# Performance work log

Hardware: AMD Instinct MI355X
Metric: run time of the kernel (lower is better)

Reference implementation:

```python
import jax, jax.numpy as jnp
import numpy as np

N_PAPER, N_AUTHOR = 200000, 100000
D_PAPER, D_AUTHOR = 128, 64
H, OUT = 64, 32
E_CITES, E_WRITES = 4000000, 2000000


def _gcn(x, W, b, src, dst, n):
    # GCNConv with default add_self_loops=True, symmetric normalization
    xl = x @ W
    deg = jnp.zeros((n,), xl.dtype).at[dst].add(1.0) + 1.0  # +1 for self loop
    dis = jax.lax.rsqrt(deg)
    norm = dis[src] * dis[dst]
    out = jax.ops.segment_sum(xl[src] * norm[:, None], dst, num_segments=n)
    out = out + xl * (dis * dis)[:, None]  # self-loop term: norm_ii = 1/deg_i
    return out + b


def _sage(x_src, x_dst, Wl, bl, Wr, src, dst, n_dst):
    # SAGEConv: mean neighbor aggregation -> lin_l, plus root lin_r on dst
    ones = jnp.ones(src.shape, x_src.dtype)
    cnt = jnp.maximum(jax.ops.segment_sum(ones, dst, num_segments=n_dst), 1.0)
    mean = jax.ops.segment_sum(x_src[src], dst, num_segments=n_dst) / cnt[:, None]
    return mean @ Wl + bl + x_dst @ Wr


def _gat(x_src, x_dst, Ws, Wd, a_s, a_d, b, src, dst, n_dst):
    # GATConv heads=1, bipartite, add_self_loops=False, leaky_relu slope 0.2
    xs = x_src @ Ws  # [Ns, H]
    xd = x_dst @ Wd  # [Nd, H]
    a_src = xs @ a_s  # [Ns]
    a_dst = xd @ a_d  # [Nd]
    e = a_src[src] + a_dst[dst]
    e = jnp.where(e > 0, e, 0.2 * e)
    m = jax.ops.segment_max(e, dst, num_segments=n_dst)
    m = jnp.where(jnp.isfinite(m), m, 0.0)  # nodes with no in-edges
    ex = jnp.exp(e - m[dst])
    denom = jax.ops.segment_sum(ex, dst, num_segments=n_dst)
    alpha = ex / denom[dst]
    out = jax.ops.segment_sum(alpha[:, None] * xs[src], dst, num_segments=n_dst)
    return out + b


def _forward(x_paper, x_author, params, cites_src, cites_dst, writes_src, writes_dst):
    for (gW, gb, sWl, sbl, sWr, aWs, aWd, aas, aad, ab) in params:
        p_gcn = _gcn(x_paper, gW, gb, cites_src, cites_dst, N_PAPER)
        p_sage = _sage(x_author, x_paper, sWl, sbl, sWr, writes_src, writes_dst, N_PAPER)
        # rev_writes: paper -> author, i.e. src=writes_dst (paper), dst=writes_src (author)
        a_gat = _gat(x_paper, x_author, aWs, aWd, aas, aad, ab, writes_dst, writes_src, N_AUTHOR)
        x_paper = jax.nn.relu(p_gcn + p_sage)  # HeteroConv aggr='sum'
        x_author = jax.nn.relu(a_gat)
    return x_paper, x_author


def setup_inputs() -> dict:
    key = jax.random.key(0)
    ks = jax.random.split(key, 40)
    rn = lambda i, shp, s=0.1: jax.random.normal(ks[i], shp, jnp.float32) * s
    inp = {}
    inp['x_paper'] = rn(0, (N_PAPER, D_PAPER), 1.0)
    inp['x_author'] = rn(1, (N_AUTHOR, D_AUTHOR), 1.0)
    dims = [(D_PAPER, D_AUTHOR), (H, H)]
    i = 2
    for l, (dp, da) in enumerate(dims):
        inp[f'gcn_W{l}'] = rn(i, (dp, H)); i += 1
        inp[f'gcn_b{l}'] = jnp.zeros((H,), jnp.float32)
        inp[f'sage_Wl{l}'] = rn(i, (da, H)); i += 1
        inp[f'sage_bl{l}'] = jnp.zeros((H,), jnp.float32)
        inp[f'sage_Wr{l}'] = rn(i, (dp, H)); i += 1
        inp[f'gat_Ws{l}'] = rn(i, (dp, H)); i += 1
        inp[f'gat_Wd{l}'] = rn(i, (da, H)); i += 1
        inp[f'gat_as{l}'] = rn(i, (H,)); i += 1
        inp[f'gat_ad{l}'] = rn(i, (H,)); i += 1
        inp[f'gat_b{l}'] = jnp.zeros((H,), jnp.float32)
    inp['lin_W'] = rn(i, (H, OUT)); i += 1
    inp['lin_b'] = jnp.zeros((OUT,), jnp.float32)
    inp['cites_src'] = jax.random.randint(ks[30], (E_CITES,), 0, N_PAPER)
    inp['cites_dst'] = jax.random.randint(ks[31], (E_CITES,), 0, N_PAPER)
    inp['writes_src'] = jax.random.randint(ks[32], (E_WRITES,), 0, N_AUTHOR)
    inp['writes_dst'] = jax.random.randint(ks[33], (E_WRITES,), 0, N_PAPER)
    return inp


def reference(x_paper, x_author,
              gcn_W0, gcn_b0, sage_Wl0, sage_bl0, sage_Wr0,
              gat_Ws0, gat_Wd0, gat_as0, gat_ad0, gat_b0,
              gcn_W1, gcn_b1, sage_Wl1, sage_bl1, sage_Wr1,
              gat_Ws1, gat_Wd1, gat_as1, gat_ad1, gat_b1,
              lin_W, lin_b,
              cites_src, cites_dst, writes_src, writes_dst):
    params = [
        (gcn_W0, gcn_b0, sage_Wl0, sage_bl0, sage_Wr0, gat_Ws0, gat_Wd0, gat_as0, gat_ad0, gat_b0),
        (gcn_W1, gcn_b1, sage_Wl1, sage_bl1, sage_Wr1, gat_Ws1, gat_Wd1, gat_as1, gat_ad1, gat_b1),
    ]
    _, x_author_out = _forward(x_paper, x_author, params, cites_src, cites_dst, writes_src, writes_dst)
    return x_author_out @ lin_W + lin_b
```

## Files before the change

kernel.cpp:

```cpp
#include <hip/hip_runtime.h>
#include <hip/hip_bf16.h>

#define NP 200000
#define NA 100000
#define DP 128
#define HD 64
#define EC 4000000
#define EW 2000000
#define NSCAN (2 * NP + NA)
#define NBUCK 8
#define CAPC 64
#define CAPW 48
#define CAPA 64

typedef __hip_bfloat16 bf16;
typedef __attribute__((ext_vector_type(8))) short short8;
typedef __attribute__((ext_vector_type(4))) float f32x4;

__device__ __forceinline__ float bf2f(bf16 h) { return __bfloat162float(h); }

__device__ __forceinline__ short8 pack8(float4 a, float4 b) {
    union {
        short8 s;
        unsigned u[4];
    } r;
    __hip_bfloat162 h;
    h = __float22bfloat162_rn(float2{a.x, a.y});
    r.u[0] = *reinterpret_cast<unsigned*>(&h);
    h = __float22bfloat162_rn(float2{a.z, a.w});
    r.u[1] = *reinterpret_cast<unsigned*>(&h);
    h = __float22bfloat162_rn(float2{b.x, b.y});
    r.u[2] = *reinterpret_cast<unsigned*>(&h);
    h = __float22bfloat162_rn(float2{b.z, b.w});
    r.u[3] = *reinterpret_cast<unsigned*>(&h);
    return r.s;
}


__global__ __launch_bounds__(256) void fill_pass_kernel(const int* __restrict__ cs,
                                                        const int* __restrict__ cd,
                                                        const int* __restrict__ ws,
                                                        const int* __restrict__ wd,
                                                        int* __restrict__ CUR,
                                                        int* __restrict__ colC,
                                                        int* __restrict__ colWd,
                                                        int* __restrict__ colWa, int bucket) {
    long i = (long)blockIdx.x * 256 + threadIdx.x;
    if (i < EC) {
        int d = __builtin_nontemporal_load(&cd[i]);
        if ((int)(((long)d * NBUCK) / NP) != bucket) return;
        int s = __builtin_nontemporal_load(&cs[i]);
        int pos = atomicAdd(&CUR[d * 4], 1);
        if (pos < CAPC) colC[(size_t)d * CAPC + pos] = s;
    } else if (i < (long)EC + EW) {
        long e = i - EC;
        int d = __builtin_nontemporal_load(&wd[e]);
        int a = __builtin_nontemporal_load(&ws[e]);
        if ((int)(((long)d * NBUCK) / NP) == bucket) {
            int pos = atomicAdd(&CUR[(NP + d) * 4], 1);
            if (pos < CAPW) colWd[(size_t)d * CAPW + pos] = a;
        }
        if ((int)(((long)a * NBUCK) / NA) == bucket) {
            int pos = atomicAdd(&CUR[(2 * NP + a) * 4], 1);
            if (pos < CAPA) colWa[(size_t)a * CAPA + pos] = d;
        }
    }
}

__global__ __launch_bounds__(256) void finalize_kernel(const int* __restrict__ CUR,
                                                       float* __restrict__ dis,
                                                       float* __restrict__ invc) {
    int i = blockIdx.x * 256 + threadIdx.x;
    if (i >= NP) return;
    dis[i] = rsqrtf((float)CUR[i * 4] + 1.0f);
    invc[i] = 1.0f / fmaxf((float)CUR[(NP + i) * 4], 1.0f);
}


__global__ __launch_bounds__(256) void conv_author_kernel(const float* __restrict__ XA,
                                                          const float* __restrict__ wvec,
                                                          bf16* __restrict__ XAbf,
                                                          float* __restrict__ adst) {
    __shared__ float vs[64];
    if (threadIdx.x < 64) vs[threadIdx.x] = wvec[threadIdx.x];
    __syncthreads();
    int r = blockIdx.x * 4 + (threadIdx.x >> 6);
    int lane = threadIdx.x & 63;
    float x = XA[(size_t)r * 64 + lane];
    XAbf[(size_t)r * 64 + lane] = __float2bfloat16(x);
    float p = x * vs[lane];
#pragma unroll
    for (int o = 32; o > 0; o >>= 1) p += __shfl_xor(p, o, 64);
    if (lane == 0) adst[r] = p;
}


__global__ void wprep_kernel(const float* __restrict__ Wg, const float* __restrict__ Wl,
                             const float* __restrict__ Wr, const float* __restrict__ Ws0,
                             const float* __restrict__ Ws1, short* __restrict__ WF) {
    int bid = blockIdx.x;
    int lane = threadIdx.x;
    int q = lane & 15, g = lane >> 4;
    int m, r;
    size_t dst;
    if (bid < 16) {
        m = 0; r = bid; dst = 0;
    } else if (bid < 40) {
        m = 1; r = bid - 16; dst = 8192;
    } else if (bid < 56) {
        m = 2; r = bid - 40; dst = 20480;
    } else {
        m = 3; r = bid - 56; dst = 28672;
    }
    int ks = r >> 2, n = r & 3;
    int col = n * 16 + q;
    float v[8];
#pragma unroll
    for (int j = 0; j < 8; j++) {
        int kr = ks * 32 + g * 8 + j;
        float x;
        if (m == 0) x = Wg[(size_t)kr * 64 + col];
        else if (m == 1) x = (kr < 64) ? Wl[(size_t)kr * 64 + col] : Wr[(size_t)(kr - 64) * 64 + col];
        else if (m == 2) x = Ws0[(size_t)kr * 64 + col];
        else x = Ws1[(size_t)kr * 64 + col];
        v[j] = x;
    }
    short8 s = pack8(float4{v[0], v[1], v[2], v[3]}, float4{v[4], v[5], v[6], v[7]});
    *reinterpret_cast<short8*>(WF + dst + ((size_t)r * 64 + lane) * 8) = s;
}


template <int K, bool ABF16, bool ADOT, bool SCALE>
__global__ __launch_bounds__(256) void mfma_gemm_kernel(const void* __restrict__ Xv,
                                                        const short* __restrict__ Wf,
                                                        bf16* __restrict__ outb,
                                                        const float* __restrict__ avec,
                                                        float* __restrict__ adot,
                                                        const float* __restrict__ rowscale) {
    int tid = threadIdx.x;
    int lane = tid & 63, q = lane & 15, g = lane >> 4;
    int rw = blockIdx.x * 64 + (tid >> 6) * 16;
    int arow = rw + q;
    f32x4 acc[4];
#pragma unroll
    for (int n = 0; n < 4; n++) acc[n] = f32x4{0.f, 0.f, 0.f, 0.f};
#pragma unroll
    for (int ks = 0; ks < K / 32; ks++) {
        short8 af;
        if constexpr (ABF16) {
            af = *reinterpret_cast<const short8*>((const bf16*)Xv + (size_t)arow * K + ks * 32 +
                                                  g * 8);
        } else {
            const float* xr = (const float*)Xv + (size_t)arow * K + ks * 32 + g * 8;
            float4 a0 = *reinterpret_cast<const float4*>(xr);
            float4 a1 = *reinterpret_cast<const float4*>(xr + 4);
            af = pack8(a0, a1);
        }
#pragma unroll
        for (int n = 0; n < 4; n++) {
            short8 bfr =
                *reinterpret_cast<const short8*>(Wf + ((size_t)(ks * 4 + n) * 64 + lane) * 8);
            acc[n] = __builtin_amdgcn_mfma_f32_16x16x32_bf16(af, bfr, acc[n], 0, 0, 0);
        }
    }
    float av[4];
    if constexpr (ADOT) {
#pragma unroll
        for (int n = 0; n < 4; n++) av[n] = avec[n * 16 + q];
    }
#pragma unroll
    for (int j = 0; j < 4; j++) {
        int R = rw + g * 4 + j;
        float sc = 1.f;
        if constexpr (SCALE) sc = rowscale[R];
#pragma unroll
        for (int n = 0; n < 4; n++) {
            outb[(size_t)R * 64 + n * 16 + q] = __float2bfloat16(acc[n][j] * sc);
        }
        if constexpr (ADOT) {
            float t = acc[0][j] * av[0] + acc[1][j] * av[1] + acc[2][j] * av[2] + acc[3][j] * av[3];
            t += __shfl_xor(t, 1, 64);
            t += __shfl_xor(t, 2, 64);
            t += __shfl_xor(t, 4, 64);
            t += __shfl_xor(t, 8, 64);
            if (q == 0) adot[R] = t;
        }
    }
}


__global__ __launch_bounds__(256) void mfma_sage_kernel(const bf16* B3bf,
                                                        const float* __restrict__ XP,
                                                        const float* __restrict__ B2,
                                                        const float* __restrict__ bl,
                                                        const short* __restrict__ Wf, bf16* P1) {
    int tid = threadIdx.x;
    int lane = tid & 63, q = lane & 15, g = lane >> 4;
    int rw = blockIdx.x * 64 + (tid >> 6) * 16;
    int arow = rw + q;
    f32x4 acc[4];
#pragma unroll
    for (int n = 0; n < 4; n++) acc[n] = f32x4{0.f, 0.f, 0.f, 0.f};
#pragma unroll
    for (int ks = 0; ks < 6; ks++) {
        short8 af;
        if (ks < 2) {
            af = *reinterpret_cast<const short8*>(B3bf + (size_t)arow * 64 + ks * 32 + g * 8);
        } else {
            const float* xr = XP + (size_t)arow * DP + (ks - 2) * 32 + g * 8;
            float4 a0 = *reinterpret_cast<const float4*>(xr);
            float4 a1 = *reinterpret_cast<const float4*>(xr + 4);
            af = pack8(a0, a1);
        }
#pragma unroll
        for (int n = 0; n < 4; n++) {
            short8 bfr =
                *reinterpret_cast<const short8*>(Wf + ((size_t)(ks * 4 + n) * 64 + lane) * 8);
            acc[n] = __builtin_amdgcn_mfma_f32_16x16x32_bf16(af, bfr, acc[n], 0, 0, 0);
        }
    }
    float blv[4];
#pragma unroll
    for (int n = 0; n < 4; n++) blv[n] = bl[n * 16 + q];
#pragma unroll
    for (int j = 0; j < 4; j++) {
        int R = rw + g * 4 + j;
#pragma unroll
        for (int n = 0; n < 4; n++) {
            int col = n * 16 + q;
            float v = acc[n][j] + B2[(size_t)R * 64 + col] + blv[n];
            P1[(size_t)R * 64 + col] = __float2bfloat16(fmaxf(v, 0.f));
        }
    }
}


__global__ __launch_bounds__(256) void gcn_gather_kernel(const bf16* __restrict__ B1,
                                                         const int* __restrict__ CUR,
                                                         const int* __restrict__ colC,
                                                         const float* __restrict__ dis,
                                                         const float* __restrict__ gb,
                                                         float* __restrict__ B2) {
    int node = __builtin_amdgcn_readfirstlane(blockIdx.x * 4 + (threadIdx.x >> 6));
    unsigned lane = threadIdx.x & 63;
    int deg = min(CUR[(unsigned)node * 4], CAPC);
    unsigned cb = (unsigned)node * CAPC;
    float dd = dis[(unsigned)node];
    float acc = bf2f(B1[((unsigned)node << 6) + lane]);
    int e = 0;
    for (; e + 8 <= deg; e += 8) {
        unsigned off[8];
#pragma unroll
        for (int j = 0; j < 8; j++) off[j] = ((unsigned)colC[cb + e + j] << 6) + lane;
        float v[8];
#pragma unroll
        for (int j = 0; j < 8; j++) v[j] = bf2f(B1[off[j]]);
#pragma unroll
        for (int j = 0; j < 8; j++) acc += v[j];
    }
    for (; e + 4 <= deg; e += 4) {
        unsigned o0 = ((unsigned)colC[cb + e] << 6) + lane;
        unsigned o1 = ((unsigned)colC[cb + e + 1] << 6) + lane;
        unsigned o2 = ((unsigned)colC[cb + e + 2] << 6) + lane;
        unsigned o3 = ((unsigned)colC[cb + e + 3] << 6) + lane;
        float v0 = bf2f(B1[o0]), v1 = bf2f(B1[o1]);
        float v2 = bf2f(B1[o2]), v3 = bf2f(B1[o3]);
        acc += v0 + v1;
        acc += v2 + v3;
    }
    for (; e < deg; e++) acc += bf2f(B1[((unsigned)colC[cb + e] << 6) + lane]);
    B2[((unsigned)node << 6) + lane] = acc * dd + gb[lane];
}


__global__ __launch_bounds__(256) void sage_gather_kernel(const bf16* __restrict__ XA,
                                                          const int* __restrict__ CUR,
                                                          const int* __restrict__ colWd,
                                                          const float* __restrict__ invc,
                                                          bf16* __restrict__ B3bf) {
    int node = __builtin_amdgcn_readfirstlane(blockIdx.x * 4 + (threadIdx.x >> 6));
    unsigned lane = threadIdx.x & 63;
    int deg = min(CUR[((unsigned)NP + node) * 4], CAPW);
    unsigned cb = (unsigned)node * CAPW;
    float acc = 0.f;
    int e = 0;
    for (; e + 8 <= deg; e += 8) {
        unsigned off[8];
#pragma unroll
        for (int j = 0; j < 8; j++) off[j] = ((unsigned)colWd[cb + e + j] << 6) + lane;
        float v[8];
#pragma unroll
        for (int j = 0; j < 8; j++) v[j] = bf2f(XA[off[j]]);
#pragma unroll
        for (int j = 0; j < 8; j++) acc += v[j];
    }
    for (; e + 4 <= deg; e += 4) {
        unsigned o0 = ((unsigned)colWd[cb + e] << 6) + lane;
        unsigned o1 = ((unsigned)colWd[cb + e + 1] << 6) + lane;
        unsigned o2 = ((unsigned)colWd[cb + e + 2] << 6) + lane;
        unsigned o3 = ((unsigned)colWd[cb + e + 3] << 6) + lane;
        float v0 = bf2f(XA[o0]), v1 = bf2f(XA[o1]);
        float v2 = bf2f(XA[o2]), v3 = bf2f(XA[o3]);
        acc += v0 + v1;
        acc += v2 + v3;
    }
    for (; e < deg; e++) acc += bf2f(XA[((unsigned)colWd[cb + e] << 6) + lane]);
    B3bf[((unsigned)node << 6) + lane] = __float2bfloat16(acc * invc[(unsigned)node]);
}


__global__ void matvec64_kernel(const float* __restrict__ Wd, const float* __restrict__ ad,
                                float* __restrict__ wvec) {
    int k = threadIdx.x;
    if (k >= 64) return;
    float s = 0.f;
    for (int c = 0; c < 64; c++) s += Wd[k * 64 + c] * ad[c];
    wvec[k] = s;
}

__device__ __forceinline__ float lrelu(float v) { return v > 0.f ? v : 0.2f * v; }


__global__ __launch_bounds__(256) void gat_l0_kernel(const bf16* __restrict__ XS,
                                                     const int* __restrict__ CUR,
                                                     const int* __restrict__ colA,
                                                     const float* __restrict__ asrc,
                                                     float* __restrict__ adst,
                                                     const float* __restrict__ ab,
                                                     const float* __restrict__ wvec1) {
    int a = __builtin_amdgcn_readfirstlane(blockIdx.x * 4 + (threadIdx.x >> 6));
    unsigned lane = threadIdx.x & 63;
    int deg = min(CUR[(2u * NP + a) * 4], CAPA);
    unsigned cb = (unsigned)a * CAPA;
    float ada = adst[(unsigned)a];
    float acc = 0.f, den = 0.f;
    int e = 0;
    for (; e + 8 <= deg; e += 8) {
        unsigned p[8];
#pragma unroll
        for (int j = 0; j < 8; j++) p[j] = (unsigned)colA[cb + e + j];
        float x[8], v[8];
#pragma unroll
        for (int j = 0; j < 8; j++) x[j] = __expf(lrelu(asrc[p[j]] + ada));
#pragma unroll
        for (int j = 0; j < 8; j++) v[j] = bf2f(XS[(p[j] << 6) + lane]);
#pragma unroll
        for (int j = 0; j < 8; j++) {
            den += x[j];
            acc += x[j] * v[j];
        }
    }
    for (; e + 4 <= deg; e += 4) {
        unsigned p0 = (unsigned)colA[cb + e], p1 = (unsigned)colA[cb + e + 1];
        unsigned p2 = (unsigned)colA[cb + e + 2], p3 = (unsigned)colA[cb + e + 3];
        float x0 = __expf(lrelu(asrc[p0] + ada));
        float x1 = __expf(lrelu(asrc[p1] + ada));
        float x2 = __expf(lrelu(asrc[p2] + ada));
        float x3 = __expf(lrelu(asrc[p3] + ada));
        den += (x0 + x1) + (x2 + x3);
        acc += x0 * bf2f(XS[(p0 << 6) + lane]);
        acc += x1 * bf2f(XS[(p1 << 6) + lane]);
        acc += x2 * bf2f(XS[(p2 << 6) + lane]);
        acc += x3 * bf2f(XS[(p3 << 6) + lane]);
    }
    for (; e < deg; e++) {
        unsigned p = (unsigned)colA[cb + e];
        float x = __expf(lrelu(asrc[p] + ada));
        den += x;
        acc += x * bf2f(XS[(p << 6) + lane]);
    }
    float inv = den > 0.f ? 1.f / den : 0.f;
    float val = fmaxf(acc * inv + ab[lane], 0.f);
    float pr = val * wvec1[lane];
#pragma unroll
    for (int o = 32; o > 0; o >>= 1) pr += __shfl_xor(pr, o, 64);
    if (lane == 0) adst[(unsigned)a] = pr;
}


__global__ __launch_bounds__(256) void gat_final_kernel(const bf16* __restrict__ XS,
                                                        const int* __restrict__ CUR,
                                                        const int* __restrict__ colA,
                                                        const float* __restrict__ asrc,
                                                        const float* __restrict__ adst,
                                                        const float* __restrict__ ab,
                                                        const float* __restrict__ linW,
                                                        const float* __restrict__ linb,
                                                        float* __restrict__ out) {
    __shared__ float Ws[64 * 32];
    __shared__ float vbuf[4][64];
    __shared__ float lbs[32];
    int tid = threadIdx.x;
    for (int i = tid; i < 64 * 32; i += 256) Ws[i] = linW[i];
    if (tid < 32) lbs[tid] = linb[tid];
    __syncthreads();
    int wid = tid >> 6;
    int a = __builtin_amdgcn_readfirstlane(blockIdx.x * 4 + wid);
    unsigned lane = tid & 63;
    int deg = min(CUR[(2u * NP + a) * 4], CAPA);
    unsigned cb = (unsigned)a * CAPA;
    float ada = adst[(unsigned)a];
    float acc = 0.f, den = 0.f;
    int e = 0;
    for (; e + 8 <= deg; e += 8) {
        unsigned p[8];
#pragma unroll
        for (int j = 0; j < 8; j++) p[j] = (unsigned)colA[cb + e + j];
        float x[8], v[8];
#pragma unroll
        for (int j = 0; j < 8; j++) x[j] = __expf(lrelu(asrc[p[j]] + ada));
#pragma unroll
        for (int j = 0; j < 8; j++) v[j] = bf2f(XS[(p[j] << 6) + lane]);
#pragma unroll
        for (int j = 0; j < 8; j++) {
            den += x[j];
            acc += x[j] * v[j];
        }
    }
    for (; e + 4 <= deg; e += 4) {
        unsigned p0 = (unsigned)colA[cb + e], p1 = (unsigned)colA[cb + e + 1];
        unsigned p2 = (unsigned)colA[cb + e + 2], p3 = (unsigned)colA[cb + e + 3];
        float x0 = __expf(lrelu(asrc[p0] + ada));
        float x1 = __expf(lrelu(asrc[p1] + ada));
        float x2 = __expf(lrelu(asrc[p2] + ada));
        float x3 = __expf(lrelu(asrc[p3] + ada));
        den += (x0 + x1) + (x2 + x3);
        acc += x0 * bf2f(XS[(p0 << 6) + lane]);
        acc += x1 * bf2f(XS[(p1 << 6) + lane]);
        acc += x2 * bf2f(XS[(p2 << 6) + lane]);
        acc += x3 * bf2f(XS[(p3 << 6) + lane]);
    }
    for (; e < deg; e++) {
        unsigned p = (unsigned)colA[cb + e];
        float x = __expf(lrelu(asrc[p] + ada));
        den += x;
        acc += x * bf2f(XS[(p << 6) + lane]);
    }
    float inv = den > 0.f ? 1.f / den : 0.f;
    vbuf[wid][lane] = fmaxf(acc * inv + ab[lane], 0.f);
    __syncthreads();
    if (tid < 128) {
        int w = tid >> 5, c = tid & 31;
        int node = blockIdx.x * 4 + w;
        float s = lbs[c];
#pragma unroll
        for (int k = 0; k < 64; k++) s += vbuf[w][k] * Ws[k * 32 + c];
        out[(size_t)node * 32 + c] = s;
    }
}


static inline int cdivi(long a, long b) { return (int)((a + b - 1) / b); }

extern "C" void kernel_launch(void* const* d_in, const int* in_sizes, int n_in, void* d_out,
                              int out_size, void* d_ws, size_t ws_size, hipStream_t stream) {
    const float* x_paper = (const float*)d_in[0];
    const float* x_author = (const float*)d_in[1];
    const float* gcn_W0 = (const float*)d_in[2];
    const float* gcn_b0 = (const float*)d_in[3];
    const float* sage_Wl0 = (const float*)d_in[4];
    const float* sage_bl0 = (const float*)d_in[5];
    const float* sage_Wr0 = (const float*)d_in[6];
    const float* gat_Ws0 = (const float*)d_in[7];
    const float* gat_Wd0 = (const float*)d_in[8];
    const float* gat_as0 = (const float*)d_in[9];
    const float* gat_ad0 = (const float*)d_in[10];
    const float* gat_b0 = (const float*)d_in[11];
    const float* gat_Ws1 = (const float*)d_in[17];
    const float* gat_Wd1 = (const float*)d_in[18];
    const float* gat_as1 = (const float*)d_in[19];
    const float* gat_ad1 = (const float*)d_in[20];
    const float* gat_b1 = (const float*)d_in[21];
    const float* lin_W = (const float*)d_in[22];
    const float* lin_b = (const float*)d_in[23];
    const int* cites_src = (const int*)d_in[24];
    const int* cites_dst = (const int*)d_in[25];
    const int* writes_src = (const int*)d_in[26];
    const int* writes_dst = (const int*)d_in[27];

    float* out = (float*)d_out;

    char* base = (char*)d_ws;
    bf16* BF = (bf16*)base;
    base += (size_t)NP * 64 * 2;
    float* B2 = (float*)base;
    base += (size_t)NP * 64 * 4;
    int* colC = (int*)base;
    bf16* B3bf = (bf16*)base;
    base += (size_t)NP * CAPC * 4;
    int* colWd = (int*)base;
    base += (size_t)NP * CAPW * 4;
    int* colWa = (int*)base;
    base += (size_t)NA * CAPA * 4;
    bf16* XAbf = (bf16*)base;
    base += (size_t)NA * 64 * 2;
    int* CUR = (int*)base;
    base += (size_t)NSCAN * 4 * 4;
    float* dis_p = (float*)base;
    float* invc = dis_p + NP;
    float* asrc = invc + NP;
    float* adst = asrc + NP;
    float* wvec0 = adst + NA;
    float* wvec1 = wvec0 + 64;
    short* WF = (short*)(wvec1 + 64);

    dim3 blk(256);
    const long EMERGED = (long)EC + EW;

    hipMemsetAsync(CUR, 0, (size_t)NSCAN * 4 * 4, stream);
    matvec64_kernel<<<1, 64, 0, stream>>>(gat_Wd0, gat_ad0, wvec0);
    matvec64_kernel<<<1, 64, 0, stream>>>(gat_Wd1, gat_ad1, wvec1);
    wprep_kernel<<<64, 64, 0, stream>>>(gcn_W0, sage_Wl0, sage_Wr0, gat_Ws0, gat_Ws1, WF);

    for (int b = 0; b < NBUCK; b++) {
        fill_pass_kernel<<<cdivi(EMERGED, 256), blk, 0, stream>>>(cites_src, cites_dst,
                                                                  writes_src, writes_dst, CUR,
                                                                  colC, colWd, colWa, b);
    }
    finalize_kernel<<<cdivi(NP, 256), blk, 0, stream>>>(CUR, dis_p, invc);

    conv_author_kernel<<<NA / 4, blk, 0, stream>>>(x_author, wvec0, XAbf, adst);

    mfma_gemm_kernel<DP, false, false, true><<<NP / 64, blk, 0, stream>>>(x_paper, WF, BF,
                                                                          nullptr, nullptr,
                                                                          dis_p);
    gcn_gather_kernel<<<NP / 4, blk, 0, stream>>>(BF, CUR, colC, dis_p, gcn_b0, B2);

    sage_gather_kernel<<<NP / 4, blk, 0, stream>>>(XAbf, CUR, colWd, invc, B3bf);
    mfma_sage_kernel<<<NP / 64, blk, 0, stream>>>(B3bf, x_paper, B2, sage_bl0, WF + 8192, B3bf);

    mfma_gemm_kernel<DP, false, true, false><<<NP / 64, blk, 0, stream>>>(x_paper, WF + 20480, BF,
                                                                          gat_as0, asrc, nullptr);
    gat_l0_kernel<<<NA / 4, blk, 0, stream>>>(BF, CUR, colWa, asrc, adst, gat_b0, wvec1);

    mfma_gemm_kernel<HD, true, true, false><<<NP / 64, blk, 0, stream>>>(B3bf, WF + 28672, BF,
                                                                         gat_as1, asrc, nullptr);
    gat_final_kernel<<<NA / 4, blk, 0, stream>>>(BF, CUR, colWa, asrc, adst, gat_b1, lin_W, lin_b,
                                                 out);
}
```

Baseline: 864.6 us.

## Fuse GCN and SAGE paper gathers, halve fill passes, merge weight prep

Merges the GCN neighbor gather and the SAGE mean gather into one per-paper-node kernel that writes its SAGE result into an interleaved 128-wide bf16 buffer. The SAGE GEMM and the final GAT GEMM read and write that buffer with a stride of 128, so one launch disappears and per-node index and degree loads are shared. The two matvec launches are folded into extra blocks of the weight-prep kernel, and the number of CSR fill bucket passes drops from 8 to 4. Fewer passes means fewer full sweeps over the edge lists, but each pass handles a wider bucket, which may increase atomic contention or reduce locality in fill_pass_kernel.

```diff
diff --git a/kernel.cpp b/kernel.cpp
--- a/kernel.cpp
+++ b/kernel.cpp
@@ -8,7 +8,7 @@
 #define EC 4000000
 #define EW 2000000
 #define NSCAN (2 * NP + NA)
-#define NBUCK 8
+#define NBUCK 4
 #define CAPC 64
 #define CAPW 48
 #define CAPA 64
@@ -97,9 +97,21 @@
 
 __global__ void wprep_kernel(const float* __restrict__ Wg, const float* __restrict__ Wl,
                              const float* __restrict__ Wr, const float* __restrict__ Ws0,
-                             const float* __restrict__ Ws1, short* __restrict__ WF) {
+                             const float* __restrict__ Ws1, short* __restrict__ WF,
+                             const float* __restrict__ Wd0, const float* __restrict__ ad0,
+                             const float* __restrict__ Wd1, const float* __restrict__ ad1,
+                             float* __restrict__ wvec0, float* __restrict__ wvec1) {
     int bid = blockIdx.x;
     int lane = threadIdx.x;
+    if (bid >= 64) {
+        const float* Wd = (bid == 64) ? Wd0 : Wd1;
+        const float* ad = (bid == 64) ? ad0 : ad1;
+        float* wv = (bid == 64) ? wvec0 : wvec1;
+        float s = 0.f;
+        for (int c = 0; c < 64; c++) s += Wd[lane * 64 + c] * ad[c];
+        wv[lane] = s;
+        return;
+    }
     int q = lane & 15, g = lane >> 4;
     int m, r;
     size_t dst;
@@ -130,7 +142,7 @@
 }
 
 
-template <int K, bool ABF16, bool ADOT, bool SCALE>
+template <int K, int ASTRIDE, bool ABF16, bool ADOT, bool SCALE>
 __global__ __launch_bounds__(256) void mfma_gemm_kernel(const void* __restrict__ Xv,
                                                         const short* __restrict__ Wf,
                                                         bf16* __restrict__ outb,
@@ -148,10 +160,10 @@
     for (int ks = 0; ks < K / 32; ks++) {
         short8 af;
         if constexpr (ABF16) {
-            af = *reinterpret_cast<const short8*>((const bf16*)Xv + (size_t)arow * K + ks * 32 +
-                                                  g * 8);
+            af = *reinterpret_cast<const short8*>((const bf16*)Xv + (size_t)arow * ASTRIDE +
+                                                  ks * 32 + g * 8);
         } else {
-            const float* xr = (const float*)Xv + (size_t)arow * K + ks * 32 + g * 8;
+            const float* xr = (const float*)Xv + (size_t)arow * ASTRIDE + ks * 32 + g * 8;
             float4 a0 = *reinterpret_cast<const float4*>(xr);
             float4 a1 = *reinterpret_cast<const float4*>(xr + 4);
             af = pack8(a0, a1);
@@ -189,7 +201,7 @@
 }
 
 
-__global__ __launch_bounds__(256) void mfma_sage_kernel(const bf16* B3bf,
+__global__ __launch_bounds__(256) void mfma_sage_kernel(const bf16* B3s,
                                                         const float* __restrict__ XP,
                                                         const float* __restrict__ B2,
                                                         const float* __restrict__ bl,
@@ -205,7 +217,7 @@
     for (int ks = 0; ks < 6; ks++) {
         short8 af;
         if (ks < 2) {
-            af = *reinterpret_cast<const short8*>(B3bf + (size_t)arow * 64 + ks * 32 + g * 8);
+            af = *reinterpret_cast<const short8*>(B3s + (size_t)arow * 128 + 64 + ks * 32 + g * 8);
         } else {
             const float* xr = XP + (size_t)arow * DP + (ks - 2) * 32 + g * 8;
             float4 a0 = *reinterpret_cast<const float4*>(xr);
@@ -229,26 +241,29 @@
         for (int n = 0; n < 4; n++) {
             int col = n * 16 + q;
             float v = acc[n][j] + B2[(size_t)R * 64 + col] + blv[n];
-            P1[(size_t)R * 64 + col] = __float2bfloat16(fmaxf(v, 0.f));
-        }
-    }
-}
-
-
-__global__ __launch_bounds__(256) void gcn_gather_kernel(const bf16* __restrict__ B1,
-                                                         const int* __restrict__ CUR,
-                                                         const int* __restrict__ colC,
-                                                         const float* __restrict__ dis,
-                                                         const float* __restrict__ gb,
-                                                         float* __restrict__ B2) {
+            P1[(size_t)R * 128 + col] = __float2bfloat16(fmaxf(v, 0.f));
+        }
+    }
+}
+
+
+__global__ __launch_bounds__(256) void paper_gather_kernel(const bf16* __restrict__ B1,
+                                                           const bf16* __restrict__ XA,
+                                                           const int* __restrict__ CUR,
+                                                           const int* colC,
+                                                           const int* __restrict__ colWd,
+                                                           const float* __restrict__ dis,
+                                                           const float* __restrict__ invc,
+                                                           const float* __restrict__ gb,
+                                                           float* __restrict__ B2, bf16* B3s) {
     int node = __builtin_amdgcn_readfirstlane(blockIdx.x * 4 + (threadIdx.x >> 6));
     unsigned lane = threadIdx.x & 63;
-    int deg = min(CUR[(unsigned)node * 4], CAPC);
+    int degc = min(CUR[(unsigned)node * 4], CAPC);
     unsigned cb = (unsigned)node * CAPC;
     float dd = dis[(unsigned)node];
     float acc = bf2f(B1[((unsigned)node << 6) + lane]);
     int e = 0;
-    for (; e + 8 <= deg; e += 8) {
+    for (; e + 8 <= degc; e += 8) {
         unsigned off[8];
 #pragma unroll
         for (int j = 0; j < 8; j++) off[j] = ((unsigned)colC[cb + e + j] << 6) + lane;
@@ -258,7 +273,7 @@
 #pragma unroll
         for (int j = 0; j < 8; j++) acc += v[j];
     }
-    for (; e + 4 <= deg; e += 4) {
+    for (; e + 4 <= degc; e += 4) {
         unsigned o0 = ((unsigned)colC[cb + e] << 6) + lane;
         unsigned o1 = ((unsigned)colC[cb + e + 1] << 6) + lane;
         unsigned o2 = ((unsigned)colC[cb + e + 2] << 6) + lane;
@@ -268,55 +283,36 @@
         acc += v0 + v1;
         acc += v2 + v3;
     }
-    for (; e < deg; e++) acc += bf2f(B1[((unsigned)colC[cb + e] << 6) + lane]);
+    for (; e < degc; e++) acc += bf2f(B1[((unsigned)colC[cb + e] << 6) + lane]);
     B2[((unsigned)node << 6) + lane] = acc * dd + gb[lane];
-}
-
-
-__global__ __launch_bounds__(256) void sage_gather_kernel(const bf16* __restrict__ XA,
-                                                          const int* __restrict__ CUR,
-                                                          const int* __restrict__ colWd,
-                                                          const float* __restrict__ invc,
-                                                          bf16* __restrict__ B3bf) {
-    int node = __builtin_amdgcn_readfirstlane(blockIdx.x * 4 + (threadIdx.x >> 6));
-    unsigned lane = threadIdx.x & 63;
-    int deg = min(CUR[((unsigned)NP + node) * 4], CAPW);
-    unsigned cb = (unsigned)node * CAPW;
-    float acc = 0.f;
-    int e = 0;
-    for (; e + 8 <= deg; e += 8) {
+    int degw = min(CUR[((unsigned)NP + node) * 4], CAPW);
+    unsigned wb = (unsigned)node * CAPW;
+    float s = 0.f;
+    e = 0;
+    for (; e + 8 <= degw; e += 8) {
         unsigned off[8];
 #pragma unroll
-        for (int j = 0; j < 8; j++) off[j] = ((unsigned)colWd[cb + e + j] << 6) + lane;
+        for (int j = 0; j < 8; j++) off[j] = ((unsigned)colWd[wb + e + j] << 6) + lane;
         float v[8];
 #pragma unroll
         for (int j = 0; j < 8; j++) v[j] = bf2f(XA[off[j]]);
 #pragma unroll
-        for (int j = 0; j < 8; j++) acc += v[j];
-    }
-    for (; e + 4 <= deg; e += 4) {
-        unsigned o0 = ((unsigned)colWd[cb + e] << 6) + lane;
-        unsigned o1 = ((unsigned)colWd[cb + e + 1] << 6) + lane;
-        unsigned o2 = ((unsigned)colWd[cb + e + 2] << 6) + lane;
-        unsigned o3 = ((unsigned)colWd[cb + e + 3] << 6) + lane;
+        for (int j = 0; j < 8; j++) s += v[j];
+    }
+    for (; e + 4 <= degw; e += 4) {
+        unsigned o0 = ((unsigned)colWd[wb + e] << 6) + lane;
+        unsigned o1 = ((unsigned)colWd[wb + e + 1] << 6) + lane;
+        unsigned o2 = ((unsigned)colWd[wb + e + 2] << 6) + lane;
+        unsigned o3 = ((unsigned)colWd[wb + e + 3] << 6) + lane;
         float v0 = bf2f(XA[o0]), v1 = bf2f(XA[o1]);
         float v2 = bf2f(XA[o2]), v3 = bf2f(XA[o3]);
-        acc += v0 + v1;
-        acc += v2 + v3;
-    }
-    for (; e < deg; e++) acc += bf2f(XA[((unsigned)colWd[cb + e] << 6) + lane]);
-    B3bf[((unsigned)node << 6) + lane] = __float2bfloat16(acc * invc[(unsigned)node]);
-}
-
-
-__global__ void matvec64_kernel(const float* __restrict__ Wd, const float* __restrict__ ad,
-                                float* __restrict__ wvec) {
-    int k = threadIdx.x;
-    if (k >= 64) return;
-    float s = 0.f;
-    for (int c = 0; c < 64; c++) s += Wd[k * 64 + c] * ad[c];
-    wvec[k] = s;
-}
+        s += v0 + v1;
+        s += v2 + v3;
+    }
+    for (; e < degw; e++) s += bf2f(XA[((unsigned)colWd[wb + e] << 6) + lane]);
+    B3s[(unsigned)node * 128u + 64u + lane] = __float2bfloat16(s * invc[(unsigned)node]);
+}
+
 
 __device__ __forceinline__ float lrelu(float v) { return v > 0.f ? v : 0.2f * v; }
 
@@ -486,7 +482,7 @@
     float* B2 = (float*)base;
     base += (size_t)NP * 64 * 4;
     int* colC = (int*)base;
-    bf16* B3bf = (bf16*)base;
+    bf16* R3 = (bf16*)base;
     base += (size_t)NP * CAPC * 4;
     int* colWd = (int*)base;
     base += (size_t)NP * CAPW * 4;
@@ -508,9 +504,8 @@
     const long EMERGED = (long)EC + EW;
 
     hipMemsetAsync(CUR, 0, (size_t)NSCAN * 4 * 4, stream);
-    matvec64_kernel<<<1, 64, 0, stream>>>(gat_Wd0, gat_ad0, wvec0);
-    matvec64_kernel<<<1, 64, 0, stream>>>(gat_Wd1, gat_ad1, wvec1);
-    wprep_kernel<<<64, 64, 0, stream>>>(gcn_W0, sage_Wl0, sage_Wr0, gat_Ws0, gat_Ws1, WF);
+    wprep_kernel<<<66, 64, 0, stream>>>(gcn_W0, sage_Wl0, sage_Wr0, gat_Ws0, gat_Ws1, WF, gat_Wd0,
+                                        gat_ad0, gat_Wd1, gat_ad1, wvec0, wvec1);
 
     for (int b = 0; b < NBUCK; b++) {
         fill_pass_kernel<<<cdivi(EMERGED, 256), blk, 0, stream>>>(cites_src, cites_dst,
@@ -521,20 +516,20 @@
 
     conv_author_kernel<<<NA / 4, blk, 0, stream>>>(x_author, wvec0, XAbf, adst);
 
-    mfma_gemm_kernel<DP, false, false, true><<<NP / 64, blk, 0, stream>>>(x_paper, WF, BF,
-                                                                          nullptr, nullptr,
-                                                                          dis_p);
-    gcn_gather_kernel<<<NP / 4, blk, 0, stream>>>(BF, CUR, colC, dis_p, gcn_b0, B2);
-
-    sage_gather_kernel<<<NP / 4, blk, 0, stream>>>(XAbf, CUR, colWd, invc, B3bf);
-    mfma_sage_kernel<<<NP / 64, blk, 0, stream>>>(B3bf, x_paper, B2, sage_bl0, WF + 8192, B3bf);
-
-    mfma_gemm_kernel<DP, false, true, false><<<NP / 64, blk, 0, stream>>>(x_paper, WF + 20480, BF,
-                                                                          gat_as0, asrc, nullptr);
+    mfma_gemm_kernel<DP, DP, false, false, true><<<NP / 64, blk, 0, stream>>>(x_paper, WF, BF,
+                                                                              nullptr, nullptr,
+                                                                              dis_p);
+    paper_gather_kernel<<<NP / 4, blk, 0, stream>>>(BF, XAbf, CUR, colC, colWd, dis_p, invc,
+                                                    gcn_b0, B2, R3);
+
+    mfma_sage_kernel<<<NP / 64, blk, 0, stream>>>(R3, x_paper, B2, sage_bl0, WF + 8192, R3);
+
+    mfma_gemm_kernel<DP, DP, false, true, false><<<NP / 64, blk, 0, stream>>>(
+        x_paper, WF + 20480, BF, gat_as0, asrc, nullptr);
     gat_l0_kernel<<<NA / 4, blk, 0, stream>>>(BF, CUR, colWa, asrc, adst, gat_b0, wvec1);
 
-    mfma_gemm_kernel<HD, true, true, false><<<NP / 64, blk, 0, stream>>>(B3bf, WF + 28672, BF,
-                                                                         gat_as1, asrc, nullptr);
+    mfma_gemm_kernel<HD, 128, true, true, false><<<NP / 64, blk, 0, stream>>>(
+        R3, WF + 28672, BF, gat_as1, asrc, nullptr);
     gat_final_kernel<<<NA / 4, blk, 0, stream>>>(BF, CUR, colWa, asrc, adst, gat_b1, lin_W, lin_b,
                                                  out);
 }
```

New measurement: 842.5 us. -2.6%, faster.
